# Kernel optimization log

Measured on AMD Instinct MI355X. Metric: run time of the kernel, lower is better.

## Reference

```python
import jax, jax.numpy as jnp
import numpy as np

N_NODES = 100000
N_EDGES = 3200000
D_FEAT = 512
HIDDEN = 16
N_CLASSES = 7


def setup_inputs() -> dict:
    key = jax.random.key(0)
    k1, k2, k3, k4 = jax.random.split(key, 4)
    x = jax.random.normal(k1, (N_NODES, D_FEAT), dtype=jnp.float32)
    edge_index = jax.random.randint(k2, (2, N_EDGES), 0, N_NODES, dtype=jnp.int64)
    # Glorot-ish scaled weights
    W1 = jax.random.normal(k3, (D_FEAT, HIDDEN), dtype=jnp.float32) * (1.0 / np.sqrt(D_FEAT))
    b1 = jnp.zeros((HIDDEN,), dtype=jnp.float32)
    W2 = jax.random.normal(k4, (HIDDEN, N_CLASSES), dtype=jnp.float32) * (1.0 / np.sqrt(HIDDEN))
    b2 = jnp.zeros((N_CLASSES,), dtype=jnp.float32)
    return {"x": x, "edge_index": edge_index, "W1": W1, "b1": b1, "W2": W2, "b2": b2}


def _gcn_norm(edge_index, num_nodes):
    # Add self-loops, then symmetric normalization: D^-1/2 A D^-1/2
    loop = jnp.arange(num_nodes, dtype=edge_index.dtype)
    src = jnp.concatenate([edge_index[0], loop])
    dst = jnp.concatenate([edge_index[1], loop])
    deg = jax.ops.segment_sum(jnp.ones_like(dst, dtype=jnp.float32), dst,
                              num_segments=num_nodes)
    dinv = jnp.where(deg > 0, jax.lax.rsqrt(deg), 0.0)
    w = dinv[src] * dinv[dst]  # [E+N]
    return src, dst, w


def _gcn_conv(x, W, b, src, dst, w, num_nodes):
    h = x @ W                               # transform first (small out dim)
    m = jax.ops.segment_sum(h[src] * w[:, None], dst, num_segments=num_nodes)
    return m + b


def reference(x, edge_index, W1, b1, W2, b2):
    n = x.shape[0]
    src, dst, w = _gcn_norm(edge_index, n)
    h = jax.nn.relu(_gcn_conv(x, W1, b1, src, dst, w, n))
    # dropout is identity at inference
    logits = _gcn_conv(h, W2, b2, src, dst, w, n)
    return jax.nn.log_softmax(logits, axis=1)
```

## Files before the change

### kernel.cpp

```cpp
#include <hip/hip_runtime.h>
#include <cmath>

#define N_NODES   100000
#define N_EDGES   3200000
#define D_FEAT    512
#define HIDDEN    16
#define N_CLASSES 7

#define NCHUNK 625
#define CHUNK  5120
#define NBKT   1563
#define BCAP   2560

typedef __attribute__((ext_vector_type(4))) float  f32x4;
typedef __attribute__((ext_vector_type(8))) short  bf16x8;

__device__ __forceinline__ short f2bf(float f) {
    union { float f; unsigned u; } v; v.f = f;
    unsigned r = v.u + 0x7fffu + ((v.u >> 16) & 1u);
    return (short)(r >> 16);
}
__device__ __forceinline__ float bf2f(unsigned short s) {
    union { unsigned u; float f; } v; v.u = ((unsigned)s) << 16;
    return v.f;
}
__device__ __forceinline__ float bflo(unsigned u) {
    union { unsigned u; float f; } v; v.u = u << 16; return v.f;
}
__device__ __forceinline__ float bfhi(unsigned u) {
    union { unsigned u; float f; } v; v.u = u & 0xFFFF0000u; return v.f;
}

__global__ __launch_bounds__(1024) void k_scatterD(const int* __restrict__ src,
                                                   const int* __restrict__ dst,
                                                   unsigned* __restrict__ cnt,
                                                   unsigned* __restrict__ packed) {
    __shared__ unsigned h[NBKT];
    int t = threadIdx.x, b = blockIdx.x;
    for (int i = t; i < NBKT; i += 1024) h[i] = 0u;
    __syncthreads();
    int base = b * CHUNK;
    #pragma unroll
    for (int k = 0; k < 5; ++k)
        atomicAdd(&h[((unsigned)dst[base + k * 1024 + t]) >> 6], 1u);
    __syncthreads();
    for (int i = t; i < NBKT; i += 1024) {
        unsigned c = h[i];
        h[i] = c ? ((unsigned)i * BCAP + atomicAdd(&cnt[i], c)) : 0u;
    }
    __syncthreads();
    #pragma unroll
    for (int k = 0; k < 5; ++k) {
        int e = base + k * 1024 + t;
        unsigned d = (unsigned)dst[e];
        unsigned pos = atomicAdd(&h[d >> 6], 1u);
        packed[pos] = ((d & 63u) << 24) | (unsigned)src[e];
    }
}

__global__ __launch_bounds__(256) void k_bucket(const unsigned* __restrict__ packed,
                                                const unsigned* __restrict__ cnt,
                                                unsigned* __restrict__ deg,
                                                unsigned* __restrict__ row_start,
                                                float* __restrict__ dinv,
                                                int* __restrict__ csr_src) {
    __shared__ unsigned hh[4][64], sc[64], cur[64];
    int t = threadIdx.x, b = blockIdx.x;
    int w = t >> 6, l = t & 63;
    unsigned rs = (unsigned)b * BCAP;
    unsigned re = rs + cnt[b];
    hh[w][l] = 0u;
    __syncthreads();
    for (unsigned i = rs + t; i < re; i += 256)
        atomicAdd(&hh[w][packed[i] >> 24], 1u);
    __syncthreads();
    unsigned total = 0u;
    if (t < 64) {
        total = hh[0][t] + hh[1][t] + hh[2][t] + hh[3][t];
        sc[t] = total;
    }
    __syncthreads();
    #pragma unroll
    for (int off = 1; off < 64; off <<= 1) {
        unsigned add = (t >= off && t < 64) ? sc[t - off] : 0u;
        __syncthreads();
        if (t < 64) sc[t] += add;
        __syncthreads();
    }
    if (t < 64) {
        unsigned excl = sc[t] - total;
        int node = b * 64 + t;
        if (node < N_NODES) {
            deg[node]       = total;
            row_start[node] = rs + excl;
            dinv[node]      = rsqrtf((float)(total + 1u));
        }
        cur[t] = rs + excl;
    }
    __syncthreads();
    for (unsigned i = rs + t; i < re; i += 256) {
        unsigned p = packed[i];
        unsigned pos = atomicAdd(&cur[p >> 24], 1u);
        csr_src[pos] = (int)(p & 0xFFFFFFu);
    }
}

__global__ __launch_bounds__(256) void k_gemm1(const float* __restrict__ x,
                                               const float* __restrict__ w1,
                                               const float* __restrict__ dinv,
                                               unsigned short* __restrict__ h1p) {
    __shared__ __align__(16) short w1t[16][520];
    int tid = threadIdx.x;
    for (int idx = tid; idx < D_FEAT * HIDDEN; idx += 256) {
        int k = idx >> 4, n = idx & 15;
        w1t[n][k] = f2bf(w1[idx]);
    }
    __syncthreads();

    int lane = tid & 63, wid = tid >> 6;
    int m  = lane & 15;
    int kg = lane >> 4;

    bf16x8 bfrag[16];
    #pragma unroll
    for (int ks = 0; ks < 16; ++ks)
        bfrag[ks] = *(const bf16x8*)&w1t[m][ks * 32 + kg * 8];

    int tile = blockIdx.x * 4 + wid;
    if (tile >= (N_NODES / 16)) return;

    const f32x4* xr = (const f32x4*)(x + (size_t)(tile * 16 + m) * D_FEAT);
    f32x4 acc = {0.f, 0.f, 0.f, 0.f};
    #pragma unroll
    for (int ks = 0; ks < 16; ++ks) {
        f32x4 x0 = xr[ks * 8 + kg * 2];
        f32x4 x1 = xr[ks * 8 + kg * 2 + 1];
        bf16x8 a;
        a[0] = f2bf(x0[0]); a[1] = f2bf(x0[1]); a[2] = f2bf(x0[2]); a[3] = f2bf(x0[3]);
        a[4] = f2bf(x1[0]); a[5] = f2bf(x1[1]); a[6] = f2bf(x1[2]); a[7] = f2bf(x1[3]);
        acc = __builtin_amdgcn_mfma_f32_16x16x32_bf16(a, bfrag[ks], acc, 0, 0, 0);
    }
    size_t base = (size_t)tile * 256;
    #pragma unroll
    for (int r = 0; r < 4; ++r) {
        int rr = kg * 4 + r;
        h1p[base + rr * 16 + m] = (unsigned short)f2bf(dinv[tile * 16 + rr] * acc[r]);
    }
}

__global__ __launch_bounds__(256) void k_gather1(const int* __restrict__ csr_src,
                                                 const unsigned* __restrict__ row_start,
                                                 const unsigned* __restrict__ deg,
                                                 const unsigned short* __restrict__ h1p,
                                                 const float* __restrict__ dinv,
                                                 const float* __restrict__ w2,
                                                 const float* __restrict__ b1,
                                                 float* __restrict__ h2p) {
    __shared__ float w2s[16][8];
    __shared__ float b1s[16];
    int tid  = threadIdx.x;
    if (tid < 128) {
        int jj = tid >> 3, c = tid & 7;
        w2s[jj][c] = (c < N_CLASSES) ? w2[jj * N_CLASSES + c] : 0.f;
    }
    if (tid < 16) b1s[tid] = b1[tid];
    __syncthreads();

    int lane = tid & 63;
    int node = blockIdx.x * 4 + (tid >> 6);
    int half = lane & 1;
    int slot = lane >> 1;

    unsigned start = row_start[node];
    unsigned end   = start + deg[node];

    float acc[8] = {0,0,0,0,0,0,0,0};
    uint4 sv = *(const uint4*)(h1p + (size_t)node * 16 + half * 8);
    if (lane < 2) {
        acc[0] += bflo(sv.x); acc[1] += bfhi(sv.x);
        acc[2] += bflo(sv.y); acc[3] += bfhi(sv.y);
        acc[4] += bflo(sv.z); acc[5] += bfhi(sv.z);
        acc[6] += bflo(sv.w); acc[7] += bfhi(sv.w);
    }
    for (unsigned e0 = start; e0 < end; e0 += 32) {
        unsigned idx = e0 + (unsigned)slot;
        if (idx < end) {
            int s = csr_src[idx];
            uint4 rv = *(const uint4*)(h1p + (size_t)s * 16 + half * 8);
            acc[0] += bflo(rv.x); acc[1] += bfhi(rv.x);
            acc[2] += bflo(rv.y); acc[3] += bfhi(rv.y);
            acc[4] += bflo(rv.z); acc[5] += bfhi(rv.z);
            acc[6] += bflo(rv.w); acc[7] += bfhi(rv.w);
        }
    }
    #pragma unroll
    for (int mk = 2; mk <= 32; mk <<= 1) {
        #pragma unroll
        for (int k = 0; k < 8; ++k) acc[k] += __shfl_xor(acc[k], mk);
    }
    float oth[8];
    #pragma unroll
    for (int k = 0; k < 8; ++k) oth[k] = __shfl_xor(acc[k], 1);

    float di = dinv[node];
    float h[16];
    #pragma unroll
    for (int k = 0; k < 8; ++k) {
        float glo = half ? oth[k] : acc[k];
        float ghi = half ? acc[k] : oth[k];
        h[k]     = fmaxf(fmaf(di, glo, b1s[k]),     0.f);
        h[k + 8] = fmaxf(fmaf(di, ghi, b1s[k + 8]), 0.f);
    }
    int c = lane & 7;
    float o = 0.f;
    #pragma unroll
    for (int j = 0; j < 16; ++j) o = fmaf(h[j], w2s[j][c], o);
    if (lane < 8)
        h2p[(size_t)node * 8 + c] = (c < N_CLASSES) ? di * o : 0.f;
}

__global__ __launch_bounds__(256) void k_gather2(const int* __restrict__ csr_src,
                                                 const unsigned* __restrict__ row_start,
                                                 const unsigned* __restrict__ deg,
                                                 const float* __restrict__ dinv,
                                                 const float* __restrict__ h2p,
                                                 const float* __restrict__ b2,
                                                 float* __restrict__ out) {
    int tid  = threadIdx.x;
    int lane = tid & 63;
    int node = blockIdx.x * 4 + (tid >> 6);
    int half = lane & 1;
    int slot = lane >> 1;

    unsigned start = row_start[node];
    unsigned end   = start + deg[node];

    float acc[4] = {0, 0, 0, 0};
    f32x4 sv = *(const f32x4*)(h2p + (size_t)node * 8 + half * 4);
    if (lane < 2) { acc[0] += sv[0]; acc[1] += sv[1]; acc[2] += sv[2]; acc[3] += sv[3]; }
    for (unsigned e0 = start; e0 < end; e0 += 32) {
        unsigned idx = e0 + (unsigned)slot;
        if (idx < end) {
            int s = csr_src[idx];
            f32x4 rv = *(const f32x4*)(h2p + (size_t)s * 8 + half * 4);
            acc[0] += rv[0]; acc[1] += rv[1]; acc[2] += rv[2]; acc[3] += rv[3];
        }
    }
    #pragma unroll
    for (int mk = 2; mk <= 32; mk <<= 1) {
        #pragma unroll
        for (int k = 0; k < 4; ++k) acc[k] += __shfl_xor(acc[k], mk);
    }
    float oth[4];
    #pragma unroll
    for (int k = 0; k < 4; ++k) oth[k] = __shfl_xor(acc[k], 1);

    float l[8];
    #pragma unroll
    for (int k = 0; k < 4; ++k) {
        l[k]     = half ? oth[k] : acc[k];
        l[k + 4] = half ? acc[k] : oth[k];
    }
    float di = dinv[node];
    float lg[N_CLASSES];
    float mx = -1e30f;
    #pragma unroll
    for (int cc = 0; cc < N_CLASSES; ++cc) {
        lg[cc] = fmaf(di, l[cc], b2[cc]);
        mx = fmaxf(mx, lg[cc]);
    }
    float sum = 0.f;
    #pragma unroll
    for (int cc = 0; cc < N_CLASSES; ++cc) sum += __expf(lg[cc] - mx);
    float lse = mx + __logf(sum);
    if (lane < N_CLASSES) {
        float v = lg[0];
        #pragma unroll
        for (int cc = 1; cc < N_CLASSES; ++cc) if (lane == cc) v = lg[cc];
        out[(size_t)node * N_CLASSES + lane] = v - lse;
    }
}

extern "C" void kernel_launch(void* const* d_in, const int* in_sizes, int n_in,
                              void* d_out, int out_size, void* d_ws, size_t ws_size,
                              hipStream_t stream) {
    const float* x  = (const float*)d_in[0];
    const int*   ei = (const int*)d_in[1];
    const float* w1 = (const float*)d_in[2];
    const float* b1 = (const float*)d_in[3];
    const float* w2 = (const float*)d_in[4];
    const float* b2 = (const float*)d_in[5];
    float* out = (float*)d_out;

    const int* src = ei;
    const int* dst = ei + N_EDGES;

    unsigned* w32            = (unsigned*)d_ws;
    float*    dinv           = (float*)(w32 + 0);
    unsigned short* h1p      = (unsigned short*)(w32 + 102400);
    float*    h2p            = (float*)(w32 + 902400);
    unsigned* deg            = w32 + 1702400;
    unsigned* row_start      = w32 + 1804800;
    unsigned* cnt            = w32 + 1907200;
    unsigned* packed         = w32 + 1909248;
    int*      csr_src        = (int*)(w32 + 5910528);

    const int GB = (N_NODES / 16 + 3) / 4;

    hipMemsetAsync(cnt, 0, NBKT * sizeof(unsigned), stream);
    k_scatterD<<<NCHUNK, 1024, 0, stream>>>(src, dst, cnt, packed);
    k_bucket  <<<NBKT,   256,  0, stream>>>(packed, cnt, deg, row_start, dinv, csr_src);
    k_gemm1   <<<GB,     256,  0, stream>>>(x, w1, dinv, h1p);
    k_gather1 <<<25000,  256,  0, stream>>>(csr_src, row_start, deg, h1p, dinv, w2, b1, h2p);
    k_gather2 <<<25000,  256,  0, stream>>>(csr_src, row_start, deg, dinv, h2p, b2, out);
}
```

Measured before the change: 496.5 us.

## Merge GEMM into edge-scatter kernel and apply degree scaling in bucket pass

The dense x@W1 MFMA GEMM now runs as extra blocks of the edge-scatter kernel, so the bandwidth-heavy read of x overlaps with the atomic-heavy edge bucketing in one launch. The GEMM writes raw fp32 results to a new workspace buffer. The bucket kernel, which computes the inverse-sqrt degrees, then scales those results and converts them to bf16. This removes one launch and the dependency of the GEMM on dinv, at the cost of an extra fp32 round trip of the 100k x 16 intermediate and 1024-thread GEMM blocks that reread W1 from LDS every step.

```diff
diff --git a/kernel.cpp b/kernel.cpp
--- a/kernel.cpp
+++ b/kernel.cpp
@@ -11,6 +11,7 @@
 #define CHUNK  5120
 #define NBKT   1563
 #define BCAP   2560
+#define GEMMB  391
 
 typedef __attribute__((ext_vector_type(4))) float  f32x4;
 typedef __attribute__((ext_vector_type(8))) short  bf16x8;
@@ -31,40 +32,79 @@
     union { unsigned u; float f; } v; v.u = u & 0xFFFF0000u; return v.f;
 }
 
-__global__ __launch_bounds__(1024) void k_scatterD(const int* __restrict__ src,
-                                                   const int* __restrict__ dst,
-                                                   unsigned* __restrict__ cnt,
-                                                   unsigned* __restrict__ packed) {
+__global__ __launch_bounds__(1024) void k_fused1(const int* __restrict__ src,
+                                                 const int* __restrict__ dst,
+                                                 unsigned* __restrict__ cnt,
+                                                 unsigned* __restrict__ packed,
+                                                 const float* __restrict__ x,
+                                                 const float* __restrict__ w1,
+                                                 float* __restrict__ graw) {
+    __shared__ __align__(16) short w1t[16][520];
     __shared__ unsigned h[NBKT];
-    int t = threadIdx.x, b = blockIdx.x;
-    for (int i = t; i < NBKT; i += 1024) h[i] = 0u;
-    __syncthreads();
-    int base = b * CHUNK;
-    #pragma unroll
-    for (int k = 0; k < 5; ++k)
-        atomicAdd(&h[((unsigned)dst[base + k * 1024 + t]) >> 6], 1u);
-    __syncthreads();
-    for (int i = t; i < NBKT; i += 1024) {
-        unsigned c = h[i];
-        h[i] = c ? ((unsigned)i * BCAP + atomicAdd(&cnt[i], c)) : 0u;
-    }
-    __syncthreads();
-    #pragma unroll
-    for (int k = 0; k < 5; ++k) {
-        int e = base + k * 1024 + t;
-        unsigned d = (unsigned)dst[e];
-        unsigned pos = atomicAdd(&h[d >> 6], 1u);
-        packed[pos] = ((d & 63u) << 24) | (unsigned)src[e];
+    int t = threadIdx.x;
+
+    if (blockIdx.x < NCHUNK) {
+        int b = blockIdx.x;
+        for (int i = t; i < NBKT; i += 1024) h[i] = 0u;
+        __syncthreads();
+        int base = b * CHUNK;
+        #pragma unroll
+        for (int k = 0; k < 5; ++k)
+            atomicAdd(&h[((unsigned)dst[base + k * 1024 + t]) >> 6], 1u);
+        __syncthreads();
+        for (int i = t; i < NBKT; i += 1024) {
+            unsigned c = h[i];
+            h[i] = c ? ((unsigned)i * BCAP + atomicAdd(&cnt[i], c)) : 0u;
+        }
+        __syncthreads();
+        #pragma unroll
+        for (int k = 0; k < 5; ++k) {
+            int e = base + k * 1024 + t;
+            unsigned d = (unsigned)dst[e];
+            unsigned pos = atomicAdd(&h[d >> 6], 1u);
+            packed[pos] = ((d & 63u) << 24) | (unsigned)src[e];
+        }
+    } else {
+        for (int idx = t; idx < D_FEAT * HIDDEN; idx += 1024) {
+            int k = idx >> 4, n = idx & 15;
+            w1t[n][k] = f2bf(w1[idx]);
+        }
+        __syncthreads();
+        int lane = t & 63, wid = t >> 6;
+        int m  = lane & 15;
+        int kg = lane >> 4;
+        int tile = (blockIdx.x - NCHUNK) * 16 + wid;
+        if (tile >= (N_NODES / 16)) return;
+
+        const f32x4* xr = (const f32x4*)(x + (size_t)(tile * 16 + m) * D_FEAT);
+        f32x4 acc = {0.f, 0.f, 0.f, 0.f};
+        #pragma unroll
+        for (int ks = 0; ks < 16; ++ks) {
+            f32x4 x0 = xr[ks * 8 + kg * 2];
+            f32x4 x1 = xr[ks * 8 + kg * 2 + 1];
+            bf16x8 a;
+            a[0] = f2bf(x0[0]); a[1] = f2bf(x0[1]); a[2] = f2bf(x0[2]); a[3] = f2bf(x0[3]);
+            a[4] = f2bf(x1[0]); a[5] = f2bf(x1[1]); a[6] = f2bf(x1[2]); a[7] = f2bf(x1[3]);
+            bf16x8 bb = *(const bf16x8*)&w1t[m][ks * 32 + kg * 8];
+            acc = __builtin_amdgcn_mfma_f32_16x16x32_bf16(a, bb, acc, 0, 0, 0);
+        }
+        size_t base = (size_t)tile * 256;
+        #pragma unroll
+        for (int r = 0; r < 4; ++r)
+            graw[base + (kg * 4 + r) * 16 + m] = acc[r];
     }
 }
 
 __global__ __launch_bounds__(256) void k_bucket(const unsigned* __restrict__ packed,
                                                 const unsigned* __restrict__ cnt,
+                                                const float* __restrict__ graw,
                                                 unsigned* __restrict__ deg,
                                                 unsigned* __restrict__ row_start,
                                                 float* __restrict__ dinv,
-                                                int* __restrict__ csr_src) {
+                                                int* __restrict__ csr_src,
+                                                unsigned short* __restrict__ h1p) {
     __shared__ unsigned hh[4][64], sc[64], cur[64];
+    __shared__ float dls[64];
     int t = threadIdx.x, b = blockIdx.x;
     int w = t >> 6, l = t & 63;
     unsigned rs = (unsigned)b * BCAP;
@@ -90,61 +130,28 @@
     if (t < 64) {
         unsigned excl = sc[t] - total;
         int node = b * 64 + t;
+        float di = rsqrtf((float)(total + 1u));
+        dls[t] = di;
         if (node < N_NODES) {
             deg[node]       = total;
             row_start[node] = rs + excl;
-            dinv[node]      = rsqrtf((float)(total + 1u));
+            dinv[node]      = di;
         }
         cur[t] = rs + excl;
     }
     __syncthreads();
+    #pragma unroll
+    for (int k = 0; k < 4; ++k) {
+        int i = t + k * 256;
+        int node = b * 64 + (i >> 4);
+        if (node < N_NODES)
+            h1p[(size_t)b * 1024 + i] =
+                (unsigned short)f2bf(dls[i >> 4] * graw[(size_t)b * 1024 + i]);
+    }
     for (unsigned i = rs + t; i < re; i += 256) {
         unsigned p = packed[i];
         unsigned pos = atomicAdd(&cur[p >> 24], 1u);
         csr_src[pos] = (int)(p & 0xFFFFFFu);
-    }
-}
-
-__global__ __launch_bounds__(256) void k_gemm1(const float* __restrict__ x,
-                                               const float* __restrict__ w1,
-                                               const float* __restrict__ dinv,
-                                               unsigned short* __restrict__ h1p) {
-    __shared__ __align__(16) short w1t[16][520];
-    int tid = threadIdx.x;
-    for (int idx = tid; idx < D_FEAT * HIDDEN; idx += 256) {
-        int k = idx >> 4, n = idx & 15;
-        w1t[n][k] = f2bf(w1[idx]);
-    }
-    __syncthreads();
-
-    int lane = tid & 63, wid = tid >> 6;
-    int m  = lane & 15;
-    int kg = lane >> 4;
-
-    bf16x8 bfrag[16];
-    #pragma unroll
-    for (int ks = 0; ks < 16; ++ks)
-        bfrag[ks] = *(const bf16x8*)&w1t[m][ks * 32 + kg * 8];
-
-    int tile = blockIdx.x * 4 + wid;
-    if (tile >= (N_NODES / 16)) return;
-
-    const f32x4* xr = (const f32x4*)(x + (size_t)(tile * 16 + m) * D_FEAT);
-    f32x4 acc = {0.f, 0.f, 0.f, 0.f};
-    #pragma unroll
-    for (int ks = 0; ks < 16; ++ks) {
-        f32x4 x0 = xr[ks * 8 + kg * 2];
-        f32x4 x1 = xr[ks * 8 + kg * 2 + 1];
-        bf16x8 a;
-        a[0] = f2bf(x0[0]); a[1] = f2bf(x0[1]); a[2] = f2bf(x0[2]); a[3] = f2bf(x0[3]);
-        a[4] = f2bf(x1[0]); a[5] = f2bf(x1[1]); a[6] = f2bf(x1[2]); a[7] = f2bf(x1[3]);
-        acc = __builtin_amdgcn_mfma_f32_16x16x32_bf16(a, bfrag[ks], acc, 0, 0, 0);
-    }
-    size_t base = (size_t)tile * 256;
-    #pragma unroll
-    for (int r = 0; r < 4; ++r) {
-        int rr = kg * 4 + r;
-        h1p[base + rr * 16 + m] = (unsigned short)f2bf(dinv[tile * 16 + rr] * acc[r]);
     }
 }
 
@@ -302,15 +309,13 @@
     unsigned* deg            = w32 + 1702400;
     unsigned* row_start      = w32 + 1804800;
     unsigned* cnt            = w32 + 1907200;
-    unsigned* packed         = w32 + 1909248;
-    int*      csr_src        = (int*)(w32 + 5910528);
-
-    const int GB = (N_NODES / 16 + 3) / 4;
+    float*    graw           = (float*)(w32 + 1909248);
+    unsigned* packed         = w32 + 3509248;
+    int*      csr_src        = (int*)(w32 + 7510528);
 
     hipMemsetAsync(cnt, 0, NBKT * sizeof(unsigned), stream);
-    k_scatterD<<<NCHUNK, 1024, 0, stream>>>(src, dst, cnt, packed);
-    k_bucket  <<<NBKT,   256,  0, stream>>>(packed, cnt, deg, row_start, dinv, csr_src);
-    k_gemm1   <<<GB,     256,  0, stream>>>(x, w1, dinv, h1p);
-    k_gather1 <<<25000,  256,  0, stream>>>(csr_src, row_start, deg, h1p, dinv, w2, b1, h2p);
-    k_gather2 <<<25000,  256,  0, stream>>>(csr_src, row_start, deg, dinv, h2p, b2, out);
-}
+    k_fused1 <<<NCHUNK + GEMMB, 1024, 0, stream>>>(src, dst, cnt, packed, x, w1, graw);
+    k_bucket <<<NBKT,  256, 0, stream>>>(packed, cnt, graw, deg, row_start, dinv, csr_src, h1p);
+    k_gather1<<<25000, 256, 0, stream>>>(csr_src, row_start, deg, h1p, dinv, w2, b1, h2p);
+    k_gather2<<<25000, 256, 0, stream>>>(csr_src, row_start, deg, dinv, h2p, b2, out);
+}
```

After: 478.4 us. 1.04x faster.
